# Performance work log

Hardware: AMD Instinct MI355X
Metric: run time of the kernel (lower is better)

The kernel has to match this reference:

```python
import jax, jax.numpy as jnp
import numpy as np

D_MODEL = 768
D_FF = 3072
N_BEHAVIORS = 4
EPS = 1e-12


def layer_norm(x, g, b):
    m = jnp.mean(x, axis=-1, keepdims=True)
    v = jnp.mean(jnp.square(x - m), axis=-1, keepdims=True)
    return (x - m) * jax.lax.rsqrt(v + EPS) * g + b


def setup_inputs() -> dict:
    key = jax.random.key(0)
    ks = jax.random.split(key, 8)
    B, L = 8, 2048
    s1 = 1.0 / np.sqrt(D_MODEL)
    s2 = 1.0 / np.sqrt(D_FF)
    return {
        "input_tensor": jax.random.normal(ks[0], (B, L, D_MODEL), dtype=jnp.float32),
        "type_seq": jax.random.randint(ks[1], (B, L), 0, N_BEHAVIORS + 1),
        # per-behavior FeedForward params, stacked on leading n dim
        "W1": jax.random.normal(ks[2], (N_BEHAVIORS, D_MODEL, D_FF), dtype=jnp.float32) * s1,
        "b1": jnp.zeros((N_BEHAVIORS, D_FF), dtype=jnp.float32),
        "W2": jax.random.normal(ks[3], (N_BEHAVIORS, D_FF, D_MODEL), dtype=jnp.float32) * s2,
        "b2": jnp.zeros((N_BEHAVIORS, D_MODEL), dtype=jnp.float32),
        "ln_g": jnp.ones((N_BEHAVIORS, D_MODEL), dtype=jnp.float32),
        "ln_b": jnp.zeros((N_BEHAVIORS, D_MODEL), dtype=jnp.float32),
        # outer LayerNorm params
        "out_g": jnp.ones((D_MODEL,), dtype=jnp.float32),
        "out_b": jnp.zeros((D_MODEL,), dtype=jnp.float32),
    }


def reference(input_tensor, type_seq, W1, b1, W2, b2, ln_g, ln_b, out_g, out_b):
    n = W1.shape[0]
    # run every behavior's FeedForward over the full sequence (dense over-compute)
    h = jnp.einsum('BLH,nHF->nBLF', input_tensor, W1) + b1[:, None, None, :]
    h = jax.nn.gelu(h, approximate=False)  # torch 'gelu' = exact erf form
    h = jnp.einsum('nBLF,nFH->nBLH', h, W2) + b2[:, None, None, :]
    # per-expert residual LayerNorm (FeedForward with residual=True)
    h = layer_norm(h + input_tensor[None], ln_g[:, None, None, :], ln_b[:, None, None, :])
    # prepend zeros branch (class 0 = padding) then one-hot select per token
    stacked = jnp.concatenate([jnp.zeros_like(input_tensor)[None], h], axis=0)  # [n+1,B,L,H]
    onehot = jax.nn.one_hot(type_seq, n + 1, dtype=input_tensor.dtype)  # [B,L,n+1]
    sel = jnp.einsum('nBLH,BLn->BLH', stacked, onehot)
    # dropout is identity in eval; fused residual + LayerNorm
    return layer_norm(sel + input_tensor, out_g, out_b)
```

## Files before the change

### kernel.cpp

```cpp
#include <hip/hip_runtime.h>
#include <hip/hip_bf16.h>
#include <math.h>

#define NTOK   16384
#define DM     768
#define DF     3072
#define NEXP   4

#define XBLKS  6144
#define W1BLKS 2304
#define W2BLKS 2304
#define PREP_BLKS (1 + XBLKS + W1BLKS + W2BLKS)

typedef short bf16x8 __attribute__((ext_vector_type(8)));
typedef float f32x4  __attribute__((ext_vector_type(4)));

#define WS_CNT    0u
#define WS_BASES  256u
#define WS_POS    512u
#define WS_LIST   (512u + 65536u)
#define WS_XB     (WS_LIST + 262144u)
#define WS_W1T    (WS_XB + 25165824u)
#define WS_W2T    (WS_W1T + 18874368u)
#define WS_H1     (WS_W2T + 18874368u)
#define WS_H2     (WS_H1 + 100663296u)
#define WS_END    (WS_H2 + 25165824u)

__device__ __forceinline__ ushort f2bf(float f) {
    unsigned int v; __builtin_memcpy(&v, &f, 4);
    v = v + 0x7fffu + ((v >> 16) & 1u);
    return (ushort)(v >> 16);
}
__device__ __forceinline__ float bf2f(ushort u) {
    unsigned int v = ((unsigned int)u) << 16;
    float f; __builtin_memcpy(&f, &v, 4); return f;
}

__device__ __forceinline__ float fast_gelu(float v) {
    float y = v + 0.044715f * v * v * v;
    float e = __builtin_amdgcn_exp2f(-2.3022082f * y);
    return v * __builtin_amdgcn_rcpf(1.0f + e);
}

typedef __attribute__((address_space(1))) const void gvoid_t;
typedef __attribute__((address_space(3))) void lvoid_t;
__device__ __forceinline__ void cp16(const void* g, void* l) {
    __builtin_amdgcn_global_load_lds((gvoid_t*)g, (lvoid_t*)l, 16, 0, 0);
}

__device__ __forceinline__ int xcd_remap(int id, int T) {
    const int q = T >> 3, r = T & 7;
    const int x = id & 7, j = id >> 3;
    return (x < r ? x * (q + 1) : r * (q + 1) + (x - r) * q) + j;
}

__device__ __forceinline__ void transpose_tile(
    const float* __restrict__ src, ushort* __restrict__ dst, int R, int C,
    int bx, int by, int tid, ushort* tile ) {
    const int r0 = by * 64, c0 = bx * 64;
#pragma unroll
    for (int q = 0; q < 2; ++q) {
        int li = q * 256 + tid;
        int r = li >> 3, c = (li & 7) * 8;
        const float* s = src + (size_t)(r0 + r) * C + (c0 + c);
        float4 v0 = *(const float4*)s;
        float4 v1 = *(const float4*)(s + 4);
        ushort tmp[8];
        tmp[0] = f2bf(v0.x); tmp[1] = f2bf(v0.y); tmp[2] = f2bf(v0.z); tmp[3] = f2bf(v0.w);
        tmp[4] = f2bf(v1.x); tmp[5] = f2bf(v1.y); tmp[6] = f2bf(v1.z); tmp[7] = f2bf(v1.w);
        int sw = (((c >> 3) ^ ((r >> 3) & 7)) << 3);
        *(uint4*)&tile[r * 72 + sw] = *(uint4*)tmp;
    }
    __syncthreads();
#pragma unroll
    for (int q = 0; q < 2; ++q) {
        int li = q * 256 + tid;
        int r = li >> 3, c = (li & 7) * 8;
        ushort tmp[8];
#pragma unroll
        for (int j = 0; j < 8; ++j)
            tmp[j] = tile[(c + j) * 72 +
                          ((((r >> 3) & 7) ^ (((c + j) >> 3) & 7)) << 3) + (r & 7)];
        *(uint4*)(dst + (size_t)(c0 + r) * R + (r0 + c)) = *(uint4*)tmp;
    }
}

__global__ __launch_bounds__(256) void prep_kernel(
    const int* __restrict__ type_seq, const float* __restrict__ X,
    const float* __restrict__ W1, const float* __restrict__ W2,
    int* __restrict__ cnt, int* __restrict__ bases,
    int* __restrict__ pos_of, int* __restrict__ list,
    ushort* __restrict__ Xb, ushort* __restrict__ W1t, ushort* __restrict__ W2t) {
    __shared__ ushort tile[64 * 72];
    __shared__ int lcnt[NEXP];
    const int tid = threadIdx.x;
    const int bid = blockIdx.x;

    if (bid == 0) {
        if (tid < NEXP) lcnt[tid] = 0;
        __syncthreads();
        const int lane = tid & 63;
        for (int it = 0; it < NTOK / 256; ++it) {
            int t = it * 256 + tid;
            int k = type_seq[t];
#pragma unroll
            for (int e = 0; e < NEXP; ++e) {
                unsigned long long m = __ballot(k == e + 1);
                int total = __popcll(m);
                int b = 0;
                if (lane == 0 && total) b = atomicAdd(&lcnt[e], total);
                b = __shfl(b, 0, 64);
                if (k == e + 1) {
                    int p = b + __popcll(m & ((1ull << lane) - 1ull));
                    list[e * NTOK + p] = t;
                    pos_of[t] = p;
                }
            }
        }
        __syncthreads();
        if (tid == 0) {
            int s = 0, mb = 0;
            for (int e = 0; e < NEXP; ++e) {
                cnt[e] = lcnt[e];
                bases[e] = s;
                bases[8 + e] = mb;
                s += lcnt[e];
                mb += (lcnt[e] + 127) >> 7;
            }
            bases[12] = mb;
        }
        return;
    }

    int id = bid - 1;
    if (id < XBLKS) {
        size_t i = (size_t)(id * 256 + tid) * 8;
        float4 v0 = *(const float4*)(X + i);
        float4 v1 = *(const float4*)(X + i + 4);
        ushort tmp[8];
        tmp[0] = f2bf(v0.x); tmp[1] = f2bf(v0.y); tmp[2] = f2bf(v0.z); tmp[3] = f2bf(v0.w);
        tmp[4] = f2bf(v1.x); tmp[5] = f2bf(v1.y); tmp[6] = f2bf(v1.z); tmp[7] = f2bf(v1.w);
        *(uint4*)(Xb + i) = *(uint4*)tmp;
        return;
    }
    id -= XBLKS;
    if (id < W1BLKS) {
        int z = id / 576, r = id % 576;
        size_t mb = (size_t)z * DM * DF;
        transpose_tile(W1 + mb, W1t + mb, DM, DF, r % 48, r / 48, tid, tile);
        return;
    }
    id -= W1BLKS;
    {
        int z = id / 576, r = id % 576;
        size_t mb = (size_t)z * DF * DM;
        transpose_tile(W2 + mb, W2t + mb, DF, DM, r % 12, r / 12, tid, tile);
    }
}


__global__ __launch_bounds__(512, 4) void gemm1_kernel(
    const ushort* __restrict__ Xb, const ushort* __restrict__ W1t,
    const float* __restrict__ b1, const int* __restrict__ cnt,
    const int* __restrict__ bases, const int* __restrict__ list,
    ushort* __restrict__ h1) {
    const int mb = bases[12];
    const int T = mb * 24;
    int id = blockIdx.y * 24 + blockIdx.x;
    if (id >= T) return;
    id = xcd_remap(id, T);
    const int y = id / 24;
    const int n0 = (id % 24) * 128;
    const int* mboff = bases + 8;
    const int e = (y >= mboff[1]) + (y >= mboff[2]) + (y >= mboff[3]);
    const int m0 = (y - mboff[e]) << 7;
    const int count = cnt[e];
    const int NK = DM / 32;

    __shared__ __align__(16) short As[3][4096];
    __shared__ __align__(16) short Bs[3][4096];

    const int tid = threadIdx.x;
    const int wave = tid >> 6, lane = tid & 63;
    const int wm = (wave & 1) * 64, wn = (wave >> 1) * 32;
    const int lrow = lane & 15;
    const int qg = lane >> 4;

    int r0 = min(m0 + (tid >> 2), count - 1);
    int t0 = list[e * NTOK + r0];
    const int qsrc = ((tid & 3) ^ ((tid >> 3) & 3)) * 8;
    const ushort* a0 = Xb + (size_t)t0 * DM + qsrc;
    const ushort* Wb = W1t + (size_t)e * DF * DM;
    const ushort* bp0 = Wb + (size_t)(n0 + (tid >> 2)) * DM + qsrc;

    int aOff[4], bOff[2];
#pragma unroll
    for (int i = 0; i < 4; ++i) {
        int ra = wm + i * 16 + lrow;
        aOff[i] = ra * 32 + (qg ^ ((ra >> 1) & 3)) * 8;
    }
#pragma unroll
    for (int j = 0; j < 2; ++j) {
        int rb = wn + j * 16 + lrow;
        bOff[j] = rb * 32 + (qg ^ ((rb >> 1) & 3)) * 8;
    }

    f32x4 z = {0.f, 0.f, 0.f, 0.f};
    f32x4 acc[4][2];
#pragma unroll
    for (int i = 0; i < 4; ++i)
#pragma unroll
        for (int j = 0; j < 2; ++j) acc[i][j] = z;

    auto STAGE = [&](int wb) {
        cp16(a0, &As[0][0] + wb * 4096 + tid * 8);
        cp16(bp0, &Bs[0][0] + wb * 4096 + tid * 8);
        a0 += 32; bp0 += 32;
    };

    STAGE(0); STAGE(1);
    int rb = 0;
    for (int ks = 0; ks < NK; ++ks) {
        __builtin_amdgcn_sched_barrier(0);
        if (ks + 1 < NK) { asm volatile("s_waitcnt vmcnt(2)" ::: "memory"); }
        else             { asm volatile("s_waitcnt vmcnt(0)" ::: "memory"); }
        __builtin_amdgcn_s_barrier();
        __builtin_amdgcn_sched_barrier(0);
        if (ks + 2 < NK) {
            int wb = rb - 1; if (wb < 0) wb += 3;
            STAGE(wb);
        }
        const short* Ab = &As[0][0] + rb * 4096;
        const short* Bb = &Bs[0][0] + rb * 4096;
        bf16x8 av[4], bv[2];
#pragma unroll
        for (int i = 0; i < 4; ++i) av[i] = *(const bf16x8*)(Ab + aOff[i]);
#pragma unroll
        for (int j = 0; j < 2; ++j) bv[j] = *(const bf16x8*)(Bb + bOff[j]);
#pragma unroll
        for (int i = 0; i < 4; ++i)
#pragma unroll
            for (int j = 0; j < 2; ++j)
                acc[i][j] = __builtin_amdgcn_mfma_f32_16x16x32_bf16(av[i], bv[j], acc[i][j], 0, 0, 0);
        rb = (rb + 1 == 3) ? 0 : rb + 1;
    }

    const int base = bases[e];
    float bias[2];
#pragma unroll
    for (int nt = 0; nt < 2; ++nt)
        bias[nt] = b1[e * DF + n0 + wn + nt * 16 + lrow];
#pragma unroll
    for (int mt = 0; mt < 4; ++mt) {
        int gm = m0 + wm + mt * 16 + (lane >> 4) * 4;
#pragma unroll
        for (int nt = 0; nt < 2; ++nt) {
            int gn = n0 + wn + nt * 16 + lrow;
#pragma unroll
            for (int r = 0; r < 4; ++r) {
                int i = gm + r;
                if (i < count) {
                    float v = acc[mt][nt][r] + bias[nt];
                    h1[(size_t)(base + i) * DF + gn] = f2bf(fast_gelu(v));
                }
            }
        }
    }
}

__global__ __launch_bounds__(512, 4) void gemm2_kernel(
    const ushort* __restrict__ h1, const ushort* __restrict__ W2t,
    const float* __restrict__ b2, const int* __restrict__ cnt,
    const int* __restrict__ bases, ushort* __restrict__ h2) {
    const int mb = bases[12];
    const int T = mb * 6;
    int id = blockIdx.y * 6 + blockIdx.x;
    if (id >= T) return;
    id = xcd_remap(id, T);
    const int y = id / 6;
    const int n0 = (id % 6) * 128;
    const int* mboff = bases + 8;
    const int e = (y >= mboff[1]) + (y >= mboff[2]) + (y >= mboff[3]);
    const int m0 = (y - mboff[e]) << 7;
    const int count = cnt[e];
    const int base = bases[e];
    const int NK = DF / 32;

    __shared__ __align__(16) short As[3][4096];
    __shared__ __align__(16) short Bs[3][4096];

    const int tid = threadIdx.x;
    const int wave = tid >> 6, lane = tid & 63;
    const int wm = (wave & 1) * 64, wn = (wave >> 1) * 32;
    const int lrow = lane & 15;
    const int qg = lane >> 4;

    int r0 = min(m0 + (tid >> 2), count - 1);
    const int qsrc = ((tid & 3) ^ ((tid >> 3) & 3)) * 8;
    const ushort* a0 = h1 + (size_t)(base + r0) * DF + qsrc;
    const ushort* Wb = W2t + (size_t)e * DM * DF;
    const ushort* bp0 = Wb + (size_t)(n0 + (tid >> 2)) * DF + qsrc;

    int aOff[4], bOff[2];
#pragma unroll
    for (int i = 0; i < 4; ++i) {
        int ra = wm + i * 16 + lrow;
        aOff[i] = ra * 32 + (qg ^ ((ra >> 1) & 3)) * 8;
    }
#pragma unroll
    for (int j = 0; j < 2; ++j) {
        int rb = wn + j * 16 + lrow;
        bOff[j] = rb * 32 + (qg ^ ((rb >> 1) & 3)) * 8;
    }

    f32x4 z = {0.f, 0.f, 0.f, 0.f};
    f32x4 acc[4][2];
#pragma unroll
    for (int i = 0; i < 4; ++i)
#pragma unroll
        for (int j = 0; j < 2; ++j) acc[i][j] = z;

    auto STAGE = [&](int wb) {
        cp16(a0, &As[0][0] + wb * 4096 + tid * 8);
        cp16(bp0, &Bs[0][0] + wb * 4096 + tid * 8);
        a0 += 32; bp0 += 32;
    };

    STAGE(0); STAGE(1);
    int rb = 0;
    for (int ks = 0; ks < NK; ++ks) {
        __builtin_amdgcn_sched_barrier(0);
        if (ks + 1 < NK) { asm volatile("s_waitcnt vmcnt(2)" ::: "memory"); }
        else             { asm volatile("s_waitcnt vmcnt(0)" ::: "memory"); }
        __builtin_amdgcn_s_barrier();
        __builtin_amdgcn_sched_barrier(0);
        if (ks + 2 < NK) {
            int wb = rb - 1; if (wb < 0) wb += 3;
            STAGE(wb);
        }
        const short* Ab = &As[0][0] + rb * 4096;
        const short* Bb = &Bs[0][0] + rb * 4096;
        bf16x8 av[4], bv[2];
#pragma unroll
        for (int i = 0; i < 4; ++i) av[i] = *(const bf16x8*)(Ab + aOff[i]);
#pragma unroll
        for (int j = 0; j < 2; ++j) bv[j] = *(const bf16x8*)(Bb + bOff[j]);
#pragma unroll
        for (int i = 0; i < 4; ++i)
#pragma unroll
            for (int j = 0; j < 2; ++j)
                acc[i][j] = __builtin_amdgcn_mfma_f32_16x16x32_bf16(av[i], bv[j], acc[i][j], 0, 0, 0);
        rb = (rb + 1 == 3) ? 0 : rb + 1;
    }

    float bias[2];
#pragma unroll
    for (int nt = 0; nt < 2; ++nt)
        bias[nt] = b2[e * DM + n0 + wn + nt * 16 + lrow];
#pragma unroll
    for (int mt = 0; mt < 4; ++mt) {
        int gm = m0 + wm + mt * 16 + (lane >> 4) * 4;
#pragma unroll
        for (int nt = 0; nt < 2; ++nt) {
            int gn = n0 + wn + nt * 16 + lrow;
#pragma unroll
            for (int r = 0; r < 4; ++r) {
                int i = gm + r;
                if (i < count)
                    h2[(size_t)(base + i) * DM + gn] = f2bf(acc[mt][nt][r] + bias[nt]);
            }
        }
    }
}

__device__ __forceinline__ void block_reduce2(float& a, float& b, float* sm, int tid) {
    __syncthreads();
#pragma unroll
    for (int off = 32; off > 0; off >>= 1) {
        a += __shfl_down(a, off, 64);
        b += __shfl_down(b, off, 64);
    }
    const int wave = tid >> 6, lane = tid & 63;
    if (lane == 0) { sm[wave] = a; sm[4 + wave] = b; }
    __syncthreads();
    a = sm[0] + sm[1] + sm[2] + sm[3];
    b = sm[4] + sm[5] + sm[6] + sm[7];
}

__global__ __launch_bounds__(256) void finalize_kernel(
    const float* __restrict__ X, const int* __restrict__ type_seq,
    const int* __restrict__ pos_of, const int* __restrict__ bases,
    const ushort* __restrict__ h2,
    const float* __restrict__ ln_g, const float* __restrict__ ln_b,
    const float* __restrict__ out_g, const float* __restrict__ out_b,
    float* __restrict__ out) {
    __shared__ float sm[8];
    const int t = blockIdx.x;
    const int tid = threadIdx.x;
    const int k = type_seq[t];

    float xv[3], rv[3];
#pragma unroll
    for (int j = 0; j < 3; ++j) xv[j] = X[(size_t)t * DM + j * 256 + tid];

    if (k > 0) {
        const int e = k - 1;
        const size_t row = (size_t)(bases[e] + pos_of[t]);
        float v[3], s1 = 0.f, s2 = 0.f;
#pragma unroll
        for (int j = 0; j < 3; ++j) {
            v[j] = bf2f(h2[row * DM + j * 256 + tid]) + xv[j];
            s1 += v[j]; s2 += v[j] * v[j];
        }
        block_reduce2(s1, s2, sm, tid);
        float m = s1 * (1.f / DM);
        float inv = rsqrtf(s2 * (1.f / DM) - m * m + 1e-12f);
#pragma unroll
        for (int j = 0; j < 3; ++j) {
            int c = j * 256 + tid;
            rv[j] = (v[j] - m) * inv * ln_g[e * DM + c] + ln_b[e * DM + c];
        }
    } else {
        rv[0] = rv[1] = rv[2] = 0.f;
    }

    float w[3], s1 = 0.f, s2 = 0.f;
#pragma unroll
    for (int j = 0; j < 3; ++j) {
        w[j] = rv[j] + xv[j];
        s1 += w[j]; s2 += w[j] * w[j];
    }
    block_reduce2(s1, s2, sm, tid);
    float m = s1 * (1.f / DM);
    float inv = rsqrtf(s2 * (1.f / DM) - m * m + 1e-12f);
#pragma unroll
    for (int j = 0; j < 3; ++j) {
        int c = j * 256 + tid;
        out[(size_t)t * DM + c] = (w[j] - m) * inv * out_g[c] + out_b[c];
    }
}

extern "C" void kernel_launch(void* const* d_in, const int* in_sizes, int n_in,
                              void* d_out, int out_size, void* d_ws, size_t ws_size,
                              hipStream_t stream) {
    if (ws_size < (size_t)WS_END) return;

    const float* X     = (const float*)d_in[0];
    const int*   type  = (const int*)d_in[1];
    const float* W1    = (const float*)d_in[2];
    const float* b1    = (const float*)d_in[3];
    const float* W2    = (const float*)d_in[4];
    const float* b2    = (const float*)d_in[5];
    const float* ln_g  = (const float*)d_in[6];
    const float* ln_b  = (const float*)d_in[7];
    const float* out_g = (const float*)d_in[8];
    const float* out_b = (const float*)d_in[9];
    float* out = (float*)d_out;

    char* ws = (char*)d_ws;
    int* cnt    = (int*)(ws + WS_CNT);
    int* bases  = (int*)(ws + WS_BASES);
    int* pos_of = (int*)(ws + WS_POS);
    int* list   = (int*)(ws + WS_LIST);
    ushort* Xb  = (ushort*)(ws + WS_XB);
    ushort* W1t = (ushort*)(ws + WS_W1T);
    ushort* W2t = (ushort*)(ws + WS_W2T);
    ushort* h1  = (ushort*)(ws + WS_H1);
    ushort* h2  = (ushort*)(ws + WS_H2);

    prep_kernel<<<PREP_BLKS, 256, 0, stream>>>(type, X, W1, W2,
                                               cnt, bases, pos_of, list, Xb, W1t, W2t);
    gemm1_kernel<<<dim3(24, 132), 512, 0, stream>>>(Xb, W1t, b1, cnt, bases, list, h1);
    gemm2_kernel<<<dim3(6, 132), 512, 0, stream>>>(h1, W2t, b2, cnt, bases, h2);
    finalize_kernel<<<NTOK, 256, 0, stream>>>(X, type, pos_of, bases, h2, ln_g, ln_b, out_g, out_b, out);
}
```

Before: 419.3 us.

## Parallelize token routing across blocks and coarsen prep conversion/transpose blocks

Token routing previously ran on a single block looping over all 16384 tokens. It is now split across 64 blocks that take global slots with atomics into a zeroed counter, and a tiny scan kernel afterward computes the expert bases. The X conversion and weight transposes are coarsened so each block handles 8 chunks or tiles, cutting block count and giving more loads in flight per thread. This adds a memset and an extra kernel launch. Within-expert token order now depends on atomic ordering, so it is no longer deterministic.

```diff
diff --git a/kernel.cpp b/kernel.cpp
--- a/kernel.cpp
+++ b/kernel.cpp
@@ -7,10 +7,10 @@
 #define DF     3072
 #define NEXP   4
 
-#define XBLKS  6144
-#define W1BLKS 2304
-#define W2BLKS 2304
-#define PREP_BLKS (1 + XBLKS + W1BLKS + W2BLKS)
+#define RBLKS  64
+#define XBLKS  768
+#define WBLKS  288
+#define PREP_BLKS (RBLKS + XBLKS + 2 * WBLKS)
 
 typedef short bf16x8 __attribute__((ext_vector_type(8)));
 typedef float f32x4  __attribute__((ext_vector_type(4)));
@@ -88,73 +88,102 @@
 __global__ __launch_bounds__(256) void prep_kernel(
     const int* __restrict__ type_seq, const float* __restrict__ X,
     const float* __restrict__ W1, const float* __restrict__ W2,
-    int* __restrict__ cnt, int* __restrict__ bases,
+    int* __restrict__ cnt,
     int* __restrict__ pos_of, int* __restrict__ list,
     ushort* __restrict__ Xb, ushort* __restrict__ W1t, ushort* __restrict__ W2t) {
     __shared__ ushort tile[64 * 72];
     __shared__ int lcnt[NEXP];
+    __shared__ int lbase[NEXP];
     const int tid = threadIdx.x;
     const int bid = blockIdx.x;
 
-    if (bid == 0) {
+    if (bid < RBLKS) {
         if (tid < NEXP) lcnt[tid] = 0;
         __syncthreads();
         const int lane = tid & 63;
-        for (int it = 0; it < NTOK / 256; ++it) {
-            int t = it * 256 + tid;
-            int k = type_seq[t];
-#pragma unroll
-            for (int e = 0; e < NEXP; ++e) {
-                unsigned long long m = __ballot(k == e + 1);
-                int total = __popcll(m);
-                int b = 0;
-                if (lane == 0 && total) b = atomicAdd(&lcnt[e], total);
-                b = __shfl(b, 0, 64);
-                if (k == e + 1) {
-                    int p = b + __popcll(m & ((1ull << lane) - 1ull));
-                    list[e * NTOK + p] = t;
-                    pos_of[t] = p;
-                }
+        const int t = bid * 256 + tid;
+        const int k = type_seq[t];
+        int my_e = -1, my_p = 0;
+#pragma unroll
+        for (int e = 0; e < NEXP; ++e) {
+            unsigned long long m = __ballot(k == e + 1);
+            int total = __popcll(m);
+            int b = 0;
+            if (lane == 0 && total) b = atomicAdd(&lcnt[e], total);
+            b = __shfl(b, 0, 64);
+            if (k == e + 1) {
+                my_e = e;
+                my_p = b + __popcll(m & ((1ull << lane) - 1ull));
             }
         }
         __syncthreads();
-        if (tid == 0) {
-            int s = 0, mb = 0;
-            for (int e = 0; e < NEXP; ++e) {
-                cnt[e] = lcnt[e];
-                bases[e] = s;
-                bases[8 + e] = mb;
-                s += lcnt[e];
-                mb += (lcnt[e] + 127) >> 7;
-            }
-            bases[12] = mb;
+        if (tid < NEXP && lcnt[tid] > 0)
+            lbase[tid] = atomicAdd(&cnt[tid], lcnt[tid]);
+        __syncthreads();
+        if (my_e >= 0) {
+            int gp = lbase[my_e] + my_p;
+            list[my_e * NTOK + gp] = t;
+            pos_of[t] = gp;
         }
         return;
     }
 
-    int id = bid - 1;
+    int id = bid - RBLKS;
     if (id < XBLKS) {
-        size_t i = (size_t)(id * 256 + tid) * 8;
-        float4 v0 = *(const float4*)(X + i);
-        float4 v1 = *(const float4*)(X + i + 4);
-        ushort tmp[8];
-        tmp[0] = f2bf(v0.x); tmp[1] = f2bf(v0.y); tmp[2] = f2bf(v0.z); tmp[3] = f2bf(v0.w);
-        tmp[4] = f2bf(v1.x); tmp[5] = f2bf(v1.y); tmp[6] = f2bf(v1.z); tmp[7] = f2bf(v1.w);
-        *(uint4*)(Xb + i) = *(uint4*)tmp;
+        size_t ibase = ((size_t)id * 8 * 256 + tid) * 8;
+        float4 va[8], vb[8];
+#pragma unroll
+        for (int k = 0; k < 8; ++k) {
+            va[k] = *(const float4*)(X + ibase + (size_t)k * 2048);
+            vb[k] = *(const float4*)(X + ibase + (size_t)k * 2048 + 4);
+        }
+#pragma unroll
+        for (int k = 0; k < 8; ++k) {
+            ushort tmp[8];
+            tmp[0] = f2bf(va[k].x); tmp[1] = f2bf(va[k].y);
+            tmp[2] = f2bf(va[k].z); tmp[3] = f2bf(va[k].w);
+            tmp[4] = f2bf(vb[k].x); tmp[5] = f2bf(vb[k].y);
+            tmp[6] = f2bf(vb[k].z); tmp[7] = f2bf(vb[k].w);
+            *(uint4*)(Xb + ibase + (size_t)k * 2048) = *(uint4*)tmp;
+        }
         return;
     }
     id -= XBLKS;
-    if (id < W1BLKS) {
-        int z = id / 576, r = id % 576;
-        size_t mb = (size_t)z * DM * DF;
-        transpose_tile(W1 + mb, W1t + mb, DM, DF, r % 48, r / 48, tid, tile);
+    if (id < WBLKS) {
+#pragma unroll 1
+        for (int k = 0; k < 8; ++k) {
+            int tt = id * 8 + k;
+            int z = tt / 576, rr = tt % 576;
+            size_t mb = (size_t)z * DM * DF;
+            transpose_tile(W1 + mb, W1t + mb, DM, DF, rr % 48, rr / 48, tid, tile);
+            __syncthreads();
+        }
         return;
     }
-    id -= W1BLKS;
+    id -= WBLKS;
     {
-        int z = id / 576, r = id % 576;
-        size_t mb = (size_t)z * DF * DM;
-        transpose_tile(W2 + mb, W2t + mb, DF, DM, r % 12, r / 12, tid, tile);
+#pragma unroll 1
+        for (int k = 0; k < 8; ++k) {
+            int tt = id * 8 + k;
+            int z = tt / 576, rr = tt % 576;
+            size_t mb = (size_t)z * DF * DM;
+            transpose_tile(W2 + mb, W2t + mb, DF, DM, rr % 12, rr / 12, tid, tile);
+            __syncthreads();
+        }
+    }
+}
+
+__global__ __launch_bounds__(64) void scan_kernel(
+    const int* __restrict__ cnt, int* __restrict__ bases) {
+    if (threadIdx.x == 0) {
+        int s = 0, mb = 0;
+        for (int e = 0; e < NEXP; ++e) {
+            bases[e] = s;
+            bases[8 + e] = mb;
+            s += cnt[e];
+            mb += (cnt[e] + 127) >> 7;
+        }
+        bases[12] = mb;
     }
 }
 
@@ -468,8 +497,10 @@
     ushort* h1  = (ushort*)(ws + WS_H1);
     ushort* h2  = (ushort*)(ws + WS_H2);
 
+    hipMemsetAsync(cnt, 0, NEXP * sizeof(int), stream);
     prep_kernel<<<PREP_BLKS, 256, 0, stream>>>(type, X, W1, W2,
-                                               cnt, bases, pos_of, list, Xb, W1t, W2t);
+                                               cnt, pos_of, list, Xb, W1t, W2t);
+    scan_kernel<<<1, 64, 0, stream>>>(cnt, bases);
     gemm1_kernel<<<dim3(24, 132), 512, 0, stream>>>(Xb, W1t, b1, cnt, bases, list, h1);
     gemm2_kernel<<<dim3(6, 132), 512, 0, stream>>>(h1, W2t, b2, cnt, bases, h2);
     finalize_kernel<<<NTOK, 256, 0, stream>>>(X, type, pos_of, bases, h2, ln_g, ln_b, out_g, out_b, out);
```

Result: faster. 385.5 us (-8.1%).
